# Performance work log

Hardware: AMD Instinct MI355X
Metric: run time of the kernel (lower is better)

Reference implementation:

```python
import jax, jax.numpy as jnp
import numpy as np

N, E = 100000, 1600000
D_IN, D_H, D_OUT = 128, 256, 64


def _linear_params(k, fin, fout):
    b = 1.0 / np.sqrt(fin)
    k1, k2 = jax.random.split(k)
    W = jax.random.uniform(k1, (fout, fin), minval=-b, maxval=b, dtype=jnp.float32)
    bias = jax.random.uniform(k2, (fout,), minval=-b, maxval=b, dtype=jnp.float32)
    return W, bias


def setup_inputs() -> dict:
    key = jax.random.key(0)
    ks = jax.random.split(key, 10)
    x = jax.random.normal(ks[0], (N, D_IN), dtype=jnp.float32)
    row = jax.random.randint(ks[1], (E,), 0, N)
    col = jax.random.randint(ks[2], (E,), 0, N)
    vals = jax.random.uniform(ks[3], (E,), dtype=jnp.float32)
    W1a, b1a = _linear_params(ks[4], D_IN, D_H)
    W2a, b2a = _linear_params(ks[5], D_H, D_H)
    W1b, b1b = _linear_params(ks[6], D_H, D_H)
    W2b, b2b = _linear_params(ks[7], D_H, D_H)
    Wf1, bf1 = _linear_params(ks[8], D_H, D_H)
    Wf2, bf2 = _linear_params(ks[9], D_H, D_OUT)
    eps0 = jnp.zeros((1,), jnp.float32)
    eps1 = jnp.zeros((1,), jnp.float32)
    return {"x": x, "row": row, "col": col, "vals": vals,
            "eps0": eps0, "W1a": W1a, "b1a": b1a, "W2a": W2a, "b2a": b2a,
            "eps1": eps1, "W1b": W1b, "b1b": b1b, "W2b": W2b, "b2b": b2b,
            "Wf1": Wf1, "bf1": bf1, "Wf2": Wf2, "bf2": bf2}


def _spmm(row, col, vals, x):
    # y[i] = sum_j A[i,j] * x[j] over edges (row=i, col=j)
    msg = vals[:, None] * x[col]          # [E, d] gather
    return jax.ops.segment_sum(msg, row, num_segments=N)  # [N, d] scatter-add


def _gin_conv(x, row, col, vals, eps, W1, b1, W2, b2):
    y = _spmm(row, col, vals, x)
    h = y + (1.0 + eps) * x               # eps-residual (eps shape [1] broadcasts)
    h = jax.nn.relu(h @ W1.T + b1)
    return h @ W2.T + b2


def reference(x, row, col, vals, eps0, W1a, b1a, W2a, b2a,
              eps1, W1b, b1b, W2b, b2b, Wf1, bf1, Wf2, bf2):
    h = _gin_conv(x, row, col, vals, eps0, W1a, b1a, W2a, b2a)
    h = _gin_conv(h, row, col, vals, eps1, W1b, b1b, W2b, b2b)
    h = jax.nn.relu(h @ Wf1.T + bf1)
    # F.dropout with p=0 (default forward arg) is identity
    return h @ Wf2.T + bf2
```

## Files before the change

### kernel.cpp

```cpp
#include <hip/hip_runtime.h>
#include <cstdint>
#include <cstddef>


using h8  = __attribute__((ext_vector_type(8))) _Float16;
using us8 = __attribute__((ext_vector_type(8))) unsigned short;
using f4  = __attribute__((ext_vector_type(4))) float;

__device__ inline unsigned short f2h(float f) {
    _Float16 h = (_Float16)f;
    unsigned short u;
    __builtin_memcpy(&u, &h, 2);
    return u;
}

__device__ inline void gl_lds16(const unsigned short* src, unsigned short* dst) {
    __builtin_amdgcn_global_load_lds(
        (const __attribute__((address_space(1))) unsigned int*)src,
        (__attribute__((address_space(3))) unsigned int*)dst, 16, 0, 0);
}

__global__ __launch_bounds__(256) void k_zero(int* p, int n) {
    int i = blockIdx.x * 256 + threadIdx.x;
    if (i < n) p[i] = 0;
}

__global__ __launch_bounds__(256) void k_hist(const int* __restrict__ row,
                                              int* __restrict__ cnt, int E) {
    int e = blockIdx.x * 256 + threadIdx.x;
    if (e < E) atomicAdd(&cnt[row[e]], 1);
}

__global__ __launch_bounds__(256) void k_scan1(const int* __restrict__ cnt,
                                               int* __restrict__ base,
                                               int* __restrict__ part, int N) {
    __shared__ int sd[256];
    int t = threadIdx.x;
    int i0 = blockIdx.x * 1024 + t * 4;
    int v0 = (i0 + 0 < N) ? cnt[i0 + 0] : 0;
    int v1 = (i0 + 1 < N) ? cnt[i0 + 1] : 0;
    int v2 = (i0 + 2 < N) ? cnt[i0 + 2] : 0;
    int v3 = (i0 + 3 < N) ? cnt[i0 + 3] : 0;
    int ts = v0 + v1 + v2 + v3;
    sd[t] = ts;
    __syncthreads();
    for (int off = 1; off < 256; off <<= 1) {
        int x = (t >= off) ? sd[t - off] : 0;
        __syncthreads();
        sd[t] += x;
        __syncthreads();
    }
    int excl = sd[t] - ts;
    if (i0 + 0 < N) base[i0 + 0] = excl;
    if (i0 + 1 < N) base[i0 + 1] = excl + v0;
    if (i0 + 2 < N) base[i0 + 2] = excl + v0 + v1;
    if (i0 + 3 < N) base[i0 + 3] = excl + v0 + v1 + v2;
    if (t == 255) part[blockIdx.x] = sd[255];
}

__global__ __launch_bounds__(256) void k_scan2(int* part, int NB) {
    __shared__ int sd[256];
    int t = threadIdx.x;
    int v = (t < NB) ? part[t] : 0;
    sd[t] = v;
    __syncthreads();
    for (int off = 1; off < 256; off <<= 1) {
        int x = (t >= off) ? sd[t - off] : 0;
        __syncthreads();
        sd[t] += x;
        __syncthreads();
    }
    if (t < NB) part[t] = sd[t] - v;
}

__global__ __launch_bounds__(256) void k_scan3(int* __restrict__ base,
                                               int* __restrict__ cursor,
                                               const int* __restrict__ part,
                                               int N, int E) {
    int i = blockIdx.x * 256 + threadIdx.x;
    if (i < N) {
        int b = base[i] + part[i >> 10];
        base[i] = b;
        cursor[i] = b;
    }
    if (i == 0) base[N] = E;
}

__global__ __launch_bounds__(256) void k_scatter(const int* __restrict__ row,
                                                 const int* __restrict__ col,
                                                 const float* __restrict__ vals,
                                                 int* __restrict__ cursor,
                                                 int2* __restrict__ edges, int E) {
    int e = blockIdx.x * 256 + threadIdx.x;
    if (e < E) {
        int p = atomicAdd(&cursor[row[e]], 1);
        edges[p] = make_int2(col[e], __float_as_int(vals[e]));
    }
}

__global__ __launch_bounds__(256) void k_cvt(const float* __restrict__ x,
                                             unsigned short* __restrict__ xh, int n) {
    int i = (blockIdx.x * 256 + threadIdx.x) * 4;
    if (i < n) {
        float4 v = *(const float4*)(x + i);
        ushort4 o = {f2h(v.x), f2h(v.y), f2h(v.z), f2h(v.w)};
        *(ushort4*)(xh + i) = o;
    }
}

__device__ inline void wprep_body(const float* __restrict__ W,
                                  unsigned short* __restrict__ Wf,
                                  int K, int M, int idx) {
    int group = idx >> 9;
    int r     = idx & 511;
    int lane  = r >> 3;
    int j     = r & 7;
    int c  = group / (M / 16);
    int ct = group - c * (M / 16);
    int n = ct * 16 + (lane & 15);
    int k = c * 32 + (lane >> 4) * 8 + j;
    float w = W[(size_t)n * K + k];
    Wf[(size_t)group * 512 + (size_t)lane * 8 + j] = f2h(w);
}

__global__ __launch_bounds__(256) void k_wprep_all(
        const float* W1a, unsigned short* Q1a, const float* W2a, unsigned short* Q2a,
        const float* W1b, unsigned short* Q1b, const float* W2b, unsigned short* Q2b,
        const float* Wf1, unsigned short* Qf1, const float* Wf2, unsigned short* Qf2) {
    int b = blockIdx.x;
    const float* W; unsigned short* Q; int K, M, lb;
    if      (b < 128)  { W = W1a; Q = Q1a; K = 128; M = 256; lb = b; }
    else if (b < 384)  { W = W2a; Q = Q2a; K = 256; M = 256; lb = b - 128; }
    else if (b < 640)  { W = W1b; Q = Q1b; K = 256; M = 256; lb = b - 384; }
    else if (b < 896)  { W = W2b; Q = Q2b; K = 256; M = 256; lb = b - 640; }
    else if (b < 1152) { W = Wf1; Q = Qf1; K = 256; M = 256; lb = b - 896; }
    else               { W = Wf2; Q = Qf2; K = 256; M = 64;  lb = b - 1152; }
    wprep_body(W, Q, K, M, lb * 256 + threadIdx.x);
}

template <int DIN>
__global__ __launch_bounds__(256, 3) void k_conv(const int* __restrict__ base,
                                                 const int2* __restrict__ edges,
                                                 const unsigned short* __restrict__ Xh,
                                                 const unsigned short* __restrict__ Wq1,
                                                 const float* __restrict__ b1,
                                                 const unsigned short* __restrict__ Wq2,
                                                 const float* __restrict__ b2,
                                                 unsigned short* __restrict__ Cout,
                                                 const float* __restrict__ epsp,
                                                 int N) {
    constexpr int MH   = 256;
    constexpr int RT   = 4;
    constexpr int NCT1 = MH / 64;
    constexpr int NCH1 = DIN / 32;
    constexpr int NCH2 = MH / 32;
    constexpr int NCT2 = MH / 64;
    constexpr int HS   = 264;
    __shared__ unsigned short S[64 * HS];

    const int t    = threadIdx.x;
    const int lane = t & 63;
    const int wq   = t >> 6;
    const int r0   = blockIdx.x * 64;
    const int lm   = lane & 15;
    const int lq   = lane >> 4;
    const int kq   = lq * 8;

    const unsigned short* w1b = Wq1 + (size_t)(wq * NCT1) * 512 + (size_t)lane * 8;
    h8 wv[NCT1], wvn[NCT1];
#pragma unroll
    for (int ct = 0; ct < NCT1; ++ct)
        wv[ct] = *(const h8*)(w1b + ct * 512);

    {
        constexpr int L = DIN / 8;
        constexpr int R = 64 / L;
        constexpr int U = 8 / R;
        const int sub  = lane % L;
        const int part = lane / L;
        const float scale = 1.0f + epsp[0];

        int nb = r0 + wq * 16 + lm;
        int sv = 0, ev = 0;
        if (nb < N) { sv = base[nb]; ev = base[nb + 1]; }

        for (int j = 0; j < 16; ++j) {
            int n = r0 + wq * 16 + j;
            float acc[8];
#pragma unroll
            for (int k = 0; k < 8; ++k) acc[k] = 0.0f;
            bool valid = (n < N);
            if (valid) {
                int s = __shfl(sv, j);
                int e = __shfl(ev, j);
                for (int i0 = s; i0 < e; i0 += 64) {
                    int rem = e - i0;
                    int idx = i0 + (lane < rem ? lane : 0);
                    int2 ed = edges[idx];
                    int   ci = ed.x;
                    float vi = (lane < rem) ? __int_as_float(ed.y) : 0.0f;
                    int lim = rem < 64 ? rem : 64;
                    for (int jj = 0; jj < lim; jj += 8) {
                        int cc[U]; float vv[U];
#pragma unroll
                        for (int u = 0; u < U; ++u) {
                            int sl = jj + u * R + part;
                            cc[u] = __shfl(ci, sl);
                            vv[u] = __shfl(vi, sl);
                        }
                        h8 g[U];
#pragma unroll
                        for (int u = 0; u < U; ++u)
                            g[u] = *(const h8*)(Xh + (size_t)cc[u] * DIN + sub * 8);
#pragma unroll
                        for (int u = 0; u < U; ++u)
#pragma unroll
                            for (int k = 0; k < 8; ++k)
                                acc[k] = fmaf((float)g[u][k], vv[u], acc[k]);
                    }
                }
#pragma unroll
                for (int st = L; st < 64; st <<= 1)
#pragma unroll
                    for (int k = 0; k < 8; ++k)
                        acc[k] += __shfl_xor(acc[k], st);
            }
            if (part == 0) {
                us8 o;
                if (valid) {
                    h8 xs = *(const h8*)(Xh + (size_t)n * DIN + sub * 8);
#pragma unroll
                    for (int k = 0; k < 8; ++k)
                        o[k] = f2h(acc[k] + scale * (float)xs[k]);
                } else {
#pragma unroll
                    for (int k = 0; k < 8; ++k) o[k] = 0;
                }
                int c = sub >> 2, q = sub & 3;
                unsigned off = (unsigned)(c * 2048 + wq * 512 + q * 128
                                          + ((j ^ (sub & 7)) * 8));
                *(us8*)(S + off) = o;
            }
        }
    }
    __syncthreads();

    f4 acc[RT][NCT1];
#pragma unroll
    for (int rt = 0; rt < RT; ++rt)
#pragma unroll
        for (int ct = 0; ct < NCT1; ++ct) acc[rt][ct] = (f4){0.f, 0.f, 0.f, 0.f};

#pragma unroll
    for (int c = 0; c < NCH1; ++c) {
        if (c + 1 < NCH1) {
#pragma unroll
            for (int ct = 0; ct < NCT1; ++ct)
                wvn[ct] = *(const h8*)(w1b + ((size_t)(c + 1) * (MH / 16) + ct) * 512);
        }
        const int key = (4 * c + lq) & 7;
        h8 ah[RT];
#pragma unroll
        for (int rt = 0; rt < RT; ++rt)
            ah[rt] = *(const h8*)(S + c * 2048 + rt * 512 + lq * 128 + (lm ^ key) * 8);
#pragma unroll
        for (int ct = 0; ct < NCT1; ++ct)
#pragma unroll
            for (int rt = 0; rt < RT; ++rt)
                acc[rt][ct] = __builtin_amdgcn_mfma_f32_16x16x32_f16(ah[rt], wv[ct], acc[rt][ct], 0, 0, 0);
        if (c + 1 < NCH1) {
#pragma unroll
            for (int ct = 0; ct < NCT1; ++ct) wv[ct] = wvn[ct];
        }
    }
    __syncthreads();

#pragma unroll
    for (int ct = 0; ct < NCT1; ++ct) {
        const int col = wq * 64 + ct * 16 + lm;
        const float bv = b1[col];
#pragma unroll
        for (int rt = 0; rt < RT; ++rt) {
#pragma unroll
            for (int reg = 0; reg < 4; ++reg) {
                int rrow = rt * 16 + lq * 4 + reg;
                float v = acc[rt][ct][reg] + bv;
                v = v > 0.f ? v : 0.f;
                S[rrow * HS + col] = f2h(v);
            }
        }
    }

    const unsigned short* w2b = Wq2 + (size_t)(wq * NCT2) * 512 + (size_t)lane * 8;
    h8 wv2[NCT2], wv2n[NCT2];
#pragma unroll
    for (int ct = 0; ct < NCT2; ++ct)
        wv2[ct] = *(const h8*)(w2b + ct * 512);
    __syncthreads();

    f4 acc2[RT][NCT2];
#pragma unroll
    for (int rt = 0; rt < RT; ++rt)
#pragma unroll
        for (int ct = 0; ct < NCT2; ++ct) acc2[rt][ct] = (f4){0.f, 0.f, 0.f, 0.f};

#pragma unroll
    for (int c = 0; c < NCH2; ++c) {
        if (c + 1 < NCH2) {
#pragma unroll
            for (int ct = 0; ct < NCT2; ++ct)
                wv2n[ct] = *(const h8*)(w2b + ((size_t)(c + 1) * (MH / 16) + ct) * 512);
        }
        const int kk = c * 32 + kq;
        h8 hh[RT];
#pragma unroll
        for (int rt = 0; rt < RT; ++rt)
            hh[rt] = *(const h8*)(S + (rt * 16 + lm) * HS + kk);
#pragma unroll
        for (int ct = 0; ct < NCT2; ++ct)
#pragma unroll
            for (int rt = 0; rt < RT; ++rt)
                acc2[rt][ct] = __builtin_amdgcn_mfma_f32_16x16x32_f16(hh[rt], wv2[ct], acc2[rt][ct], 0, 0, 0);
        if (c + 1 < NCH2) {
#pragma unroll
            for (int ct = 0; ct < NCT2; ++ct) wv2[ct] = wv2n[ct];
        }
    }

#pragma unroll
    for (int ct = 0; ct < NCT2; ++ct) {
        const int col = wq * 64 + ct * 16 + lm;
        const float bv = b2[col];
#pragma unroll
        for (int rt = 0; rt < RT; ++rt) {
#pragma unroll
            for (int reg = 0; reg < 4; ++reg) {
                int n = r0 + rt * 16 + lq * 4 + reg;
                if (n < N)
                    Cout[(size_t)n * MH + col] = f2h(acc2[rt][ct][reg] + bv);
            }
        }
    }
}

template <int K, int MO>
__global__ __launch_bounds__(256, 3) void k_mlp(const unsigned short* __restrict__ A,
                                                const unsigned short* __restrict__ Wq1,
                                                const float* __restrict__ b1,
                                                const unsigned short* __restrict__ Wq2,
                                                const float* __restrict__ b2,
                                                float* __restrict__ Cv, int N) {
    constexpr int MH   = 256;
    constexpr int RT   = 4;
    constexpr int NCT1 = MH / 64;
    constexpr int NCH1 = K / 32;
    constexpr int NCH2 = MH / 32;
    constexpr int NCT2 = MO / 64 > 0 ? MO / 64 : 1;
    constexpr int HS   = 264;
    __shared__ unsigned short S[64 * HS];

    const int t    = threadIdx.x;
    const int lane = t & 63;
    const int wq   = t >> 6;
    const int r0   = blockIdx.x * 64;
    const int lm   = lane & 15;
    const int lq   = lane >> 4;
    const int kq   = lq * 8;

    int gr = r0 + wq * 16 + lm;
    if (gr >= N) gr = N - 1;
    const unsigned short* gA = A + (size_t)gr * K + kq;

    const unsigned short* w1b = Wq1 + (size_t)(wq * NCT1) * 512 + (size_t)lane * 8;
    h8 wv[NCT1], wvn[NCT1];
#pragma unroll
    for (int ct = 0; ct < NCT1; ++ct)
        wv[ct] = *(const h8*)(w1b + ct * 512);
#pragma unroll
    for (int c = 0; c < NCH1; ++c)
        gl_lds16(gA + c * 32, S + c * 2048 + wq * 512);
    __syncthreads();

    f4 acc[RT][NCT1];
#pragma unroll
    for (int rt = 0; rt < RT; ++rt)
#pragma unroll
        for (int ct = 0; ct < NCT1; ++ct) acc[rt][ct] = (f4){0.f, 0.f, 0.f, 0.f};

#pragma unroll
    for (int c = 0; c < NCH1; ++c) {
        if (c + 1 < NCH1) {
#pragma unroll
            for (int ct = 0; ct < NCT1; ++ct)
                wvn[ct] = *(const h8*)(w1b + ((size_t)(c + 1) * (MH / 16) + ct) * 512);
        }
        const unsigned short* ab = S + c * 2048;
        h8 ah[RT];
#pragma unroll
        for (int rt = 0; rt < RT; ++rt)
            ah[rt] = *(const h8*)(ab + rt * 512 + lane * 8);
#pragma unroll
        for (int ct = 0; ct < NCT1; ++ct)
#pragma unroll
            for (int rt = 0; rt < RT; ++rt)
                acc[rt][ct] = __builtin_amdgcn_mfma_f32_16x16x32_f16(ah[rt], wv[ct], acc[rt][ct], 0, 0, 0);
        if (c + 1 < NCH1) {
#pragma unroll
            for (int ct = 0; ct < NCT1; ++ct) wv[ct] = wvn[ct];
        }
    }
    __syncthreads();

#pragma unroll
    for (int ct = 0; ct < NCT1; ++ct) {
        const int col = wq * 64 + ct * 16 + lm;
        const float bv = b1[col];
#pragma unroll
        for (int rt = 0; rt < RT; ++rt) {
#pragma unroll
            for (int reg = 0; reg < 4; ++reg) {
                int rrow = rt * 16 + lq * 4 + reg;
                float v = acc[rt][ct][reg] + bv;
                v = v > 0.f ? v : 0.f;
                S[rrow * HS + col] = f2h(v);
            }
        }
    }

    const unsigned short* w2b = Wq2 + (size_t)(wq * NCT2) * 512 + (size_t)lane * 8;
    h8 wv2[NCT2], wv2n[NCT2];
#pragma unroll
    for (int ct = 0; ct < NCT2; ++ct)
        wv2[ct] = *(const h8*)(w2b + ct * 512);
    __syncthreads();

    f4 acc2[RT][NCT2];
#pragma unroll
    for (int rt = 0; rt < RT; ++rt)
#pragma unroll
        for (int ct = 0; ct < NCT2; ++ct) acc2[rt][ct] = (f4){0.f, 0.f, 0.f, 0.f};

#pragma unroll
    for (int c = 0; c < NCH2; ++c) {
        if (c + 1 < NCH2) {
#pragma unroll
            for (int ct = 0; ct < NCT2; ++ct)
                wv2n[ct] = *(const h8*)(w2b + ((size_t)(c + 1) * (MO / 16) + ct) * 512);
        }
        const int kk = c * 32 + kq;
        h8 hh[RT];
#pragma unroll
        for (int rt = 0; rt < RT; ++rt)
            hh[rt] = *(const h8*)(S + (rt * 16 + lm) * HS + kk);
#pragma unroll
        for (int ct = 0; ct < NCT2; ++ct)
#pragma unroll
            for (int rt = 0; rt < RT; ++rt)
                acc2[rt][ct] = __builtin_amdgcn_mfma_f32_16x16x32_f16(hh[rt], wv2[ct], acc2[rt][ct], 0, 0, 0);
        if (c + 1 < NCH2) {
#pragma unroll
            for (int ct = 0; ct < NCT2; ++ct) wv2[ct] = wv2n[ct];
        }
    }

#pragma unroll
    for (int ct = 0; ct < NCT2; ++ct) {
        const int col = wq * (MO / 4) + ct * 16 + lm;
        const float bv = b2[col];
#pragma unroll
        for (int rt = 0; rt < RT; ++rt) {
#pragma unroll
            for (int reg = 0; reg < 4; ++reg) {
                int n = r0 + rt * 16 + lq * 4 + reg;
                if (n < N)
                    Cv[(size_t)n * MO + col] = acc2[rt][ct][reg] + bv;
            }
        }
    }
}

extern "C" void kernel_launch(void* const* d_in, const int* in_sizes, int n_in,
                              void* d_out, int out_size, void* d_ws, size_t ws_size,
                              hipStream_t stream) {
    const float* x    = (const float*)d_in[0];
    const int*   row  = (const int*)d_in[1];
    const int*   col  = (const int*)d_in[2];
    const float* vals = (const float*)d_in[3];
    const float* eps0 = (const float*)d_in[4];
    const float* W1a  = (const float*)d_in[5];
    const float* b1a  = (const float*)d_in[6];
    const float* W2a  = (const float*)d_in[7];
    const float* b2a  = (const float*)d_in[8];
    const float* eps1 = (const float*)d_in[9];
    const float* W1b  = (const float*)d_in[10];
    const float* b1b  = (const float*)d_in[11];
    const float* W2b  = (const float*)d_in[12];
    const float* b2b  = (const float*)d_in[13];
    const float* Wf1  = (const float*)d_in[14];
    const float* bf1  = (const float*)d_in[15];
    const float* Wf2  = (const float*)d_in[16];
    const float* bf2  = (const float*)d_in[17];
    float* out = (float*)d_out;

    const int N = in_sizes[0] / 128;
    const int E = in_sizes[1];

    char* w = (char*)d_ws;
    auto alloc = [&](size_t bytes) -> void* {
        void* p = (void*)w;
        w += (bytes + 255) & ~(size_t)255;
        return p;
    };
    unsigned short* Hb1    = (unsigned short*)alloc((size_t)N * 256 * 2);
    unsigned short* Hb2    = (unsigned short*)alloc((size_t)N * 256 * 2);
    unsigned short* xh     = (unsigned short*)alloc((size_t)N * 128 * 2);
    int*            cnt    = (int*)alloc((size_t)N * 4);
    int*            basep  = (int*)alloc((size_t)(N + 1) * 4);
    int*            cursor = (int*)alloc((size_t)N * 4);
    int*            part   = (int*)alloc(1024);
    int2*           edges  = (int2*)alloc((size_t)E * 8);
    unsigned short* Wq1a = (unsigned short*)alloc((size_t)128 * 256 * 2);
    unsigned short* Wq2a = (unsigned short*)alloc((size_t)256 * 256 * 2);
    unsigned short* Wq1b = (unsigned short*)alloc((size_t)256 * 256 * 2);
    unsigned short* Wq2b = (unsigned short*)alloc((size_t)256 * 256 * 2);
    unsigned short* Wqf1 = (unsigned short*)alloc((size_t)256 * 256 * 2);
    unsigned short* Wqf2 = (unsigned short*)alloc((size_t)256 * 64 * 2);

    k_zero<<<(N + 255) / 256, 256, 0, stream>>>(cnt, N);
    k_hist<<<(E + 255) / 256, 256, 0, stream>>>(row, cnt, E);
    int nb = (N + 1023) / 1024;
    k_scan1<<<nb, 256, 0, stream>>>(cnt, basep, part, N);
    k_scan2<<<1, 256, 0, stream>>>(part, nb);
    k_scan3<<<(N + 255) / 256, 256, 0, stream>>>(basep, cursor, part, N, E);
    k_scatter<<<(E + 255) / 256, 256, 0, stream>>>(row, col, vals, cursor, edges, E);

    k_wprep_all<<<1216, 256, 0, stream>>>(W1a, Wq1a, W2a, Wq2a, W1b, Wq1b,
                                          W2b, Wq2b, Wf1, Wqf1, Wf2, Wqf2);
    k_cvt<<<(N * 128 / 4 + 255) / 256, 256, 0, stream>>>(x, xh, N * 128);

    const int grid = (N + 63) / 64;

    k_conv<128><<<grid, 256, 0, stream>>>(basep, edges, xh, Wq1a, b1a,
                                          Wq2a, b2a, Hb1, eps0, N);
    k_conv<256><<<grid, 256, 0, stream>>>(basep, edges, Hb1, Wq1b, b1b,
                                          Wq2b, b2b, Hb2, eps1, N);
    k_mlp<256, 64><<<grid, 256, 0, stream>>>(Hb2, Wqf1, bf1, Wqf2, bf2, out, N);
}
```

Baseline: 602.8 us.

## Swizzle LDS hidden tile, raise occupancy hint, merge prep kernels

Replaces the padded 64x264 LDS tile in the conv and MLP kernels with an unpadded 64x256 tile that uses an XOR swizzle on 8-element groups. This keeps bank-conflict avoidance while shrinking shared memory per block. The launch-bounds hint goes from 3 to 5 blocks per CU to raise occupancy, which risks register spills. Separately, the x conversion, count zeroing and weight prep are merged into one launch to cut kernel-launch overhead.

```diff
diff --git a/kernel.cpp b/kernel.cpp
--- a/kernel.cpp
+++ b/kernel.cpp
@@ -18,11 +18,6 @@
     __builtin_amdgcn_global_load_lds(
         (const __attribute__((address_space(1))) unsigned int*)src,
         (__attribute__((address_space(3))) unsigned int*)dst, 16, 0, 0);
-}
-
-__global__ __launch_bounds__(256) void k_zero(int* p, int n) {
-    int i = blockIdx.x * 256 + threadIdx.x;
-    if (i < n) p[i] = 0;
 }
 
 __global__ __launch_bounds__(256) void k_hist(const int* __restrict__ row,
@@ -95,16 +90,6 @@
     if (e < E) {
         int p = atomicAdd(&cursor[row[e]], 1);
         edges[p] = make_int2(col[e], __float_as_int(vals[e]));
-    }
-}
-
-__global__ __launch_bounds__(256) void k_cvt(const float* __restrict__ x,
-                                             unsigned short* __restrict__ xh, int n) {
-    int i = (blockIdx.x * 256 + threadIdx.x) * 4;
-    if (i < n) {
-        float4 v = *(const float4*)(x + i);
-        ushort4 o = {f2h(v.x), f2h(v.y), f2h(v.z), f2h(v.w)};
-        *(ushort4*)(xh + i) = o;
     }
 }
 
@@ -123,11 +108,27 @@
     Wf[(size_t)group * 512 + (size_t)lane * 8 + j] = f2h(w);
 }
 
-__global__ __launch_bounds__(256) void k_wprep_all(
+__global__ __launch_bounds__(256) void k_prep0(
+        const float* __restrict__ x, unsigned short* __restrict__ xh,
+        int* __restrict__ cnt, int N, int ncv, int nzb,
         const float* W1a, unsigned short* Q1a, const float* W2a, unsigned short* Q2a,
         const float* W1b, unsigned short* Q1b, const float* W2b, unsigned short* Q2b,
         const float* Wf1, unsigned short* Qf1, const float* Wf2, unsigned short* Qf2) {
     int b = blockIdx.x;
+    if (b < ncv) {
+        int i = (b * 256 + threadIdx.x) * 4;
+        float4 v = *(const float4*)(x + i);
+        ushort4 o = {f2h(v.x), f2h(v.y), f2h(v.z), f2h(v.w)};
+        *(ushort4*)(xh + i) = o;
+        return;
+    }
+    b -= ncv;
+    if (b < nzb) {
+        int i = b * 256 + threadIdx.x;
+        if (i < N) cnt[i] = 0;
+        return;
+    }
+    b -= nzb;
     const float* W; unsigned short* Q; int K, M, lb;
     if      (b < 128)  { W = W1a; Q = Q1a; K = 128; M = 256; lb = b; }
     else if (b < 384)  { W = W2a; Q = Q2a; K = 256; M = 256; lb = b - 128; }
@@ -139,7 +140,7 @@
 }
 
 template <int DIN>
-__global__ __launch_bounds__(256, 3) void k_conv(const int* __restrict__ base,
+__global__ __launch_bounds__(256, 5) void k_conv(const int* __restrict__ base,
                                                  const int2* __restrict__ edges,
                                                  const unsigned short* __restrict__ Xh,
                                                  const unsigned short* __restrict__ Wq1,
@@ -155,8 +156,7 @@
     constexpr int NCH1 = DIN / 32;
     constexpr int NCH2 = MH / 32;
     constexpr int NCT2 = MH / 64;
-    constexpr int HS   = 264;
-    __shared__ unsigned short S[64 * HS];
+    __shared__ unsigned short S[16384];
 
     const int t    = threadIdx.x;
     const int lane = t & 63;
@@ -279,6 +279,7 @@
     for (int ct = 0; ct < NCT1; ++ct) {
         const int col = wq * 64 + ct * 16 + lm;
         const float bv = b1[col];
+        const int g = col >> 3, wi = col & 7;
 #pragma unroll
         for (int rt = 0; rt < RT; ++rt) {
 #pragma unroll
@@ -286,7 +287,7 @@
                 int rrow = rt * 16 + lq * 4 + reg;
                 float v = acc[rt][ct][reg] + bv;
                 v = v > 0.f ? v : 0.f;
-                S[rrow * HS + col] = f2h(v);
+                S[rrow * 256 + ((g ^ (rrow & 7)) << 3) + wi] = f2h(v);
             }
         }
     }
@@ -311,11 +312,13 @@
             for (int ct = 0; ct < NCT2; ++ct)
                 wv2n[ct] = *(const h8*)(w2b + ((size_t)(c + 1) * (MH / 16) + ct) * 512);
         }
-        const int kk = c * 32 + kq;
         h8 hh[RT];
 #pragma unroll
-        for (int rt = 0; rt < RT; ++rt)
-            hh[rt] = *(const h8*)(S + (rt * 16 + lm) * HS + kk);
+        for (int rt = 0; rt < RT; ++rt) {
+            int r = rt * 16 + lm;
+            int gg = (c * 4 + lq) ^ (lm & 7);
+            hh[rt] = *(const h8*)(S + r * 256 + gg * 8);
+        }
 #pragma unroll
         for (int ct = 0; ct < NCT2; ++ct)
 #pragma unroll
@@ -344,7 +347,7 @@
 }
 
 template <int K, int MO>
-__global__ __launch_bounds__(256, 3) void k_mlp(const unsigned short* __restrict__ A,
+__global__ __launch_bounds__(256, 5) void k_mlp(const unsigned short* __restrict__ A,
                                                 const unsigned short* __restrict__ Wq1,
                                                 const float* __restrict__ b1,
                                                 const unsigned short* __restrict__ Wq2,
@@ -356,8 +359,7 @@
     constexpr int NCH1 = K / 32;
     constexpr int NCH2 = MH / 32;
     constexpr int NCT2 = MO / 64 > 0 ? MO / 64 : 1;
-    constexpr int HS   = 264;
-    __shared__ unsigned short S[64 * HS];
+    __shared__ unsigned short S[16384];
 
     const int t    = threadIdx.x;
     const int lane = t & 63;
@@ -415,6 +417,7 @@
     for (int ct = 0; ct < NCT1; ++ct) {
         const int col = wq * 64 + ct * 16 + lm;
         const float bv = b1[col];
+        const int g = col >> 3, wi = col & 7;
 #pragma unroll
         for (int rt = 0; rt < RT; ++rt) {
 #pragma unroll
@@ -422,7 +425,7 @@
                 int rrow = rt * 16 + lq * 4 + reg;
                 float v = acc[rt][ct][reg] + bv;
                 v = v > 0.f ? v : 0.f;
-                S[rrow * HS + col] = f2h(v);
+                S[rrow * 256 + ((g ^ (rrow & 7)) << 3) + wi] = f2h(v);
             }
         }
     }
@@ -447,11 +450,13 @@
             for (int ct = 0; ct < NCT2; ++ct)
                 wv2n[ct] = *(const h8*)(w2b + ((size_t)(c + 1) * (MO / 16) + ct) * 512);
         }
-        const int kk = c * 32 + kq;
         h8 hh[RT];
 #pragma unroll
-        for (int rt = 0; rt < RT; ++rt)
-            hh[rt] = *(const h8*)(S + (rt * 16 + lm) * HS + kk);
+        for (int rt = 0; rt < RT; ++rt) {
+            int r = rt * 16 + lm;
+            int gg = (c * 4 + lq) ^ (lm & 7);
+            hh[rt] = *(const h8*)(S + r * 256 + gg * 8);
+        }
 #pragma unroll
         for (int ct = 0; ct < NCT2; ++ct)
 #pragma unroll
@@ -526,7 +531,12 @@
     unsigned short* Wqf1 = (unsigned short*)alloc((size_t)256 * 256 * 2);
     unsigned short* Wqf2 = (unsigned short*)alloc((size_t)256 * 64 * 2);
 
-    k_zero<<<(N + 255) / 256, 256, 0, stream>>>(cnt, N);
+    const int ncv = (N * 128 / 4) / 256;
+    const int nzb = (N + 255) / 256;
+    k_prep0<<<ncv + nzb + 1216, 256, 0, stream>>>(
+        x, xh, cnt, N, ncv, nzb,
+        W1a, Wq1a, W2a, Wq2a, W1b, Wq1b, W2b, Wq2b, Wf1, Wqf1, Wf2, Wqf2);
+
     k_hist<<<(E + 255) / 256, 256, 0, stream>>>(row, cnt, E);
     int nb = (N + 1023) / 1024;
     k_scan1<<<nb, 256, 0, stream>>>(cnt, basep, part, N);
@@ -534,10 +544,6 @@
     k_scan3<<<(N + 255) / 256, 256, 0, stream>>>(basep, cursor, part, N, E);
     k_scatter<<<(E + 255) / 256, 256, 0, stream>>>(row, col, vals, cursor, edges, E);
 
-    k_wprep_all<<<1216, 256, 0, stream>>>(W1a, Wq1a, W2a, Wq2a, W1b, Wq1b,
-                                          W2b, Wq2b, Wf1, Wqf1, Wf2, Wqf2);
-    k_cvt<<<(N * 128 / 4 + 255) / 256, 256, 0, stream>>>(x, xh, N * 128);
-
     const int grid = (N + 63) / 64;
 
     k_conv<128><<<grid, 256, 0, stream>>>(basep, edges, xh, Wq1a, b1a,
```

Result: slower. 696.3 us (+15.5%).
